# Optimization experiments

Hardware: AMD Instinct MI355X
Metric: run time of the kernel (lower is better)

Reference implementation:

```python
import jax, jax.numpy as jnp
import numpy as np

B, N, E, H = 8, 1024, 768, 12
HD = E // H

def setup_inputs() -> dict:
    key = jax.random.key(0)
    k1, k2, k3, k4, k5 = jax.random.split(key, 5)
    s = 0.02
    return {
        'query': jax.random.normal(k1, (B, N, E), dtype=jnp.float32),
        'qkv_w': jax.random.normal(k2, (3 * E, E), dtype=jnp.float32) * s,
        'qkv_b': jax.random.normal(k3, (3 * E,), dtype=jnp.float32) * s,
        'out_w': jax.random.normal(k4, (E, E), dtype=jnp.float32) * s,
        'out_b': jax.random.normal(k5, (E,), dtype=jnp.float32) * s,
    }

def reference(query, qkv_w, qkv_b, out_w, out_b):
    b, n, e = query.shape
    scale = HD ** -0.5
    # torch Linear: x @ W^T + b
    qkv = query @ qkv_w.T + qkv_b              # [B,N,3E]
    qkv = qkv.reshape(b, n, 3, H, HD)
    q = qkv[:, :, 0].transpose(0, 2, 1, 3)     # [B,H,N,hd]
    k = qkv[:, :, 1].transpose(0, 2, 1, 3)
    v = qkv[:, :, 2].transpose(0, 2, 1, 3)
    attn = jnp.einsum('bhqd,bhkd->bhqk', q, k) * scale
    attn = jax.nn.softmax(attn, axis=-1)
    x = jnp.einsum('bhqk,bhkd->bhqd', attn, v)  # [B,H,N,hd]
    x = x.transpose(0, 2, 1, 3).reshape(b, n, e)
    return x @ out_w.T + out_b
```

## Files before the change

### kernel.cpp

```cpp
#include <hip/hip_runtime.h>
#include <cstdint>
#include <cstddef>

#define QSCALE 0.18033688011112042f

typedef __bf16 bf16x8 __attribute__((ext_vector_type(8)));
typedef __bf16 bf16x4 __attribute__((ext_vector_type(4)));
typedef short short4v __attribute__((ext_vector_type(4)));
typedef float floatx4 __attribute__((ext_vector_type(4)));

static __device__ __forceinline__ uint16_t f2bf(float f) {
    uint32_t u = __builtin_bit_cast(uint32_t, f);
    u += 0x7FFFu + ((u >> 16) & 1u);
    return (uint16_t)(u >> 16);
}

static __device__ __forceinline__ void st_bf16(uint16_t* p, float f) {
    *(__bf16*)p = (__bf16)f;
}

static __device__ __forceinline__ bf16x8 ld_frag(const uint16_t* p) {
    uint4 u = *(const uint4*)p;
    return __builtin_bit_cast(bf16x8, u);
}

static __device__ __forceinline__ void async_lds16(const uint16_t* g, uint16_t* l) {
    __builtin_amdgcn_global_load_lds(
        (const __attribute__((address_space(1))) void*)g,
        (__attribute__((address_space(3))) void*)l,
        16, 0, 0);
}

static __device__ __forceinline__ size_t qk_swz(int bh, int idx, int hd) {
    return (size_t)bh * 65536 + (size_t)(idx >> 4) * 1024 + (size_t)(hd >> 5) * 512
         + (size_t)((hd & 31) >> 3) * 128 + (size_t)(idx & 15) * 8 + (hd & 7);
}
static __device__ __forceinline__ size_t v_swz(int bh, int hd, int key) {
    return (size_t)bh * 65536 + (size_t)(key >> 6) * 4096 + (size_t)(hd >> 4) * 1024
         + (size_t)((key >> 4) & 3) * 256 + (size_t)((key >> 2) & 3) * 64
         + (size_t)(hd & 15) * 4 + (key & 3);
}

__global__ __launch_bounds__(256) void cast3_kernel(
    const float* __restrict__ a, uint16_t* __restrict__ da, int na8,
    const float* __restrict__ b, uint16_t* __restrict__ db, int nb8,
    const float* __restrict__ c, uint16_t* __restrict__ dc, int nc8)
{
    int i = blockIdx.x * 256 + threadIdx.x;
    const float* src; uint16_t* dst; int idx;
    if (i < na8)                { src = a; dst = da; idx = i; }
    else if (i < na8 + nb8)     { src = b; dst = db; idx = i - na8; }
    else if (i < na8 + nb8 + nc8){ src = c; dst = dc; idx = i - na8 - nb8; }
    else return;
    const float4* p = (const float4*)src + (size_t)2 * idx;
    float4 x = p[0], y = p[1];
    uint32_t w0 = (uint32_t)f2bf(x.x) | ((uint32_t)f2bf(x.y) << 16);
    uint32_t w1 = (uint32_t)f2bf(x.z) | ((uint32_t)f2bf(x.w) << 16);
    uint32_t w2 = (uint32_t)f2bf(y.x) | ((uint32_t)f2bf(y.y) << 16);
    uint32_t w3 = (uint32_t)f2bf(y.z) | ((uint32_t)f2bf(y.w) << 16);
    uint4 v; v.x = w0; v.y = w1; v.z = w2; v.w = w3;
    *((uint4*)dst + idx) = v;
}

__global__ __launch_bounds__(256) void gemm_qkv_kernel(
    const uint16_t* __restrict__ X,
    const uint16_t* __restrict__ W,
    const float* __restrict__ bias,
    uint16_t* __restrict__ Qs, uint16_t* __restrict__ Ks, uint16_t* __restrict__ Vs)
{
    __shared__ __align__(16) uint16_t As[128 * 32];
    __shared__ __align__(16) uint16_t Bs[128 * 32];
    const int tid = threadIdx.x;
    const int wave = tid >> 6, lane = tid & 63;
    const int L = lane & 15, quad = lane >> 4;
    const int wM = (wave >> 1) * 64, wN = (wave & 1) * 64;
    const int bm = blockIdx.x * 128;
    const int bn = blockIdx.y * 128;

    floatx4 zero4 = {0.f, 0.f, 0.f, 0.f};
    floatx4 acc[4][4];
    #pragma unroll
    for (int i = 0; i < 4; ++i)
        #pragma unroll
        for (int j = 0; j < 4; ++j) acc[i][j] = zero4;

    const int srow = tid >> 2;
    const int scol = ((tid & 3) ^ ((srow >> 1) & 3)) * 8;
    const uint16_t* xp0 = X + (size_t)(bm + srow) * 768 + scol;
    const uint16_t* xp1 = xp0 + (size_t)64 * 768;
    const uint16_t* wp0 = W + (size_t)(bn + srow) * 768 + scol;
    const uint16_t* wp1 = wp0 + (size_t)64 * 768;
    uint16_t* lA0 = As + wave * 512;
    uint16_t* lA1 = As + 2048 + wave * 512;
    uint16_t* lB0 = Bs + wave * 512;
    uint16_t* lB1 = Bs + 2048 + wave * 512;

    const int cq = (quad ^ ((L >> 1) & 3)) * 8;

    for (int k0 = 0; k0 < 768; k0 += 32) {
        __syncthreads();
        async_lds16(xp0 + k0, lA0);
        async_lds16(xp1 + k0, lA1);
        async_lds16(wp0 + k0, lB0);
        async_lds16(wp1 + k0, lB1);
        __syncthreads();
        bf16x8 af[4], bfr[4];
        #pragma unroll
        for (int mi = 0; mi < 4; ++mi) af[mi]  = ld_frag(&As[(wM + mi * 16 + L) * 32 + cq]);
        #pragma unroll
        for (int ni = 0; ni < 4; ++ni) bfr[ni] = ld_frag(&Bs[(wN + ni * 16 + L) * 32 + cq]);
        #pragma unroll
        for (int mi = 0; mi < 4; ++mi)
            #pragma unroll
            for (int ni = 0; ni < 4; ++ni)
                acc[mi][ni] = __builtin_amdgcn_mfma_f32_16x16x32_bf16(
                    af[mi], bfr[ni], acc[mi][ni], 0, 0, 0);
    }

    const int part = bn / 768;
    #pragma unroll
    for (int ni = 0; ni < 4; ++ni) {
        int col = bn + wN + ni * 16 + L;
        int c = col - part * 768;
        int h = c >> 6, hd = c & 63;
        float bv = bias[col];
        #pragma unroll
        for (int mi = 0; mi < 4; ++mi) {
            #pragma unroll
            for (int r = 0; r < 4; ++r) {
                int m = bm + wM + mi * 16 + quad * 4 + r;
                int b = m >> 10, ns = m & 1023;
                int bh = b * 12 + h;
                float v = acc[mi][ni][r] + bv;
                if (part == 0)      st_bf16(&Qs[qk_swz(bh, ns, hd)], v * QSCALE);
                else if (part == 1) st_bf16(&Ks[qk_swz(bh, ns, hd)], v);
                else                st_bf16(&Vs[v_swz(bh, hd, ns)], v);
            }
        }
    }
}

__global__ __launch_bounds__(256) void attn_kernel(
    const uint16_t* __restrict__ Qs,
    const uint16_t* __restrict__ Ks,
    const uint16_t* __restrict__ Vs,
    uint16_t* __restrict__ Ob)
{
    __shared__ __align__(16) uint16_t Ksh[4096];
    __shared__ __align__(16) uint16_t Vsh[4096];
    const int tid = threadIdx.x;
    const int wave = tid >> 6, lane = tid & 63;
    const int L = lane & 15, quad = lane >> 4;
    const int bh = blockIdx.x;
    const int qt = blockIdx.y;
    const int b = bh / 12, h = bh - b * 12;
    const int q0 = qt * 128 + wave * 32;

    floatx4 zero4 = {0.f, 0.f, 0.f, 0.f};

    const uint16_t* qbase = Qs + (size_t)bh * 65536 + (size_t)lane * 8;
    bf16x8 aq[2][2];
    #pragma unroll
    for (int st = 0; st < 2; ++st) {
        const uint16_t* qp = qbase + (size_t)(qt * 8 + wave * 2 + st) * 1024;
        aq[st][0] = ld_frag(qp);
        aq[st][1] = ld_frag(qp + 512);
    }

    floatx4 accO[2][4];
    #pragma unroll
    for (int st = 0; st < 2; ++st)
        #pragma unroll
        for (int t = 0; t < 4; ++t) accO[st][t] = zero4;
    float lacc[2] = {0.f, 0.f};

    const uint16_t* ktile0 = Ks + (size_t)bh * 65536;
    const uint16_t* vtile0 = Vs + (size_t)bh * 65536;
    const size_t lane8 = (size_t)lane * 8;

    for (int j = 0; j < 16; ++j) {
        __syncthreads();
        const uint16_t* kt = ktile0 + (size_t)j * 4096;
        const uint16_t* vt = vtile0 + (size_t)j * 4096;
        async_lds16(kt + (size_t)wave * 512 + lane8,       Ksh + wave * 512);
        async_lds16(kt + (size_t)(wave + 4) * 512 + lane8, Ksh + (wave + 4) * 512);
        async_lds16(vt + (size_t)wave * 512 + lane8,       Vsh + wave * 512);
        async_lds16(vt + (size_t)(wave + 4) * 512 + lane8, Vsh + (wave + 4) * 512);
        __syncthreads();

        bf16x8 ka[4][2];
        #pragma unroll
        for (int kc = 0; kc < 4; ++kc) {
            ka[kc][0] = ld_frag(&Ksh[kc * 1024 + lane * 8]);
            ka[kc][1] = ld_frag(&Ksh[kc * 1024 + 512 + lane * 8]);
        }
        short4v va[4][4];
        #pragma unroll
        for (int t = 0; t < 4; ++t)
            #pragma unroll
            for (int kc = 0; kc < 4; ++kc)
                va[kc][t] = *(const short4v*)(&Vsh[t * 1024 + kc * 256 + lane * 4]);

        floatx4 c[2][4];
        #pragma unroll
        for (int st = 0; st < 2; ++st)
            #pragma unroll
            for (int kc = 0; kc < 4; ++kc) {
                floatx4 z = zero4;
                z = __builtin_amdgcn_mfma_f32_16x16x32_bf16(ka[kc][0], aq[st][0], z, 0, 0, 0);
                z = __builtin_amdgcn_mfma_f32_16x16x32_bf16(ka[kc][1], aq[st][1], z, 0, 0, 0);
                c[st][kc] = z;
            }

        short4v pb[2][4];
        #pragma unroll
        for (int st = 0; st < 2; ++st)
            #pragma unroll
            for (int kc = 0; kc < 4; ++kc) {
                float p0 = __builtin_amdgcn_exp2f(c[st][kc][0]);
                float p1 = __builtin_amdgcn_exp2f(c[st][kc][1]);
                float p2 = __builtin_amdgcn_exp2f(c[st][kc][2]);
                float p3 = __builtin_amdgcn_exp2f(c[st][kc][3]);
                lacc[st] += (p0 + p1) + (p2 + p3);
                bf16x4 t4;
                t4.x = (__bf16)p0; t4.y = (__bf16)p1;
                t4.z = (__bf16)p2; t4.w = (__bf16)p3;
                pb[st][kc] = __builtin_bit_cast(short4v, t4);
            }

        #pragma unroll
        for (int st = 0; st < 2; ++st)
            #pragma unroll
            for (int t = 0; t < 4; ++t)
                #pragma unroll
                for (int kc = 0; kc < 4; ++kc)
                    accO[st][t] = __builtin_amdgcn_mfma_f32_16x16x16bf16_1k(
                        va[kc][t], pb[st][kc], accO[st][t], 0, 0, 0);
    }

    #pragma unroll
    for (int st = 0; st < 2; ++st) {
        float sum = lacc[st];
        sum += __shfl_xor(sum, 16);
        sum += __shfl_xor(sum, 32);
        float inv = 1.f / sum;
        uint16_t* orow = Ob + ((size_t)b * 1024 + q0 + st * 16 + L) * 768 + h * 64 + quad * 4;
        #pragma unroll
        for (int t = 0; t < 4; ++t) {
            bf16x4 o4;
            o4.x = (__bf16)(accO[st][t][0] * inv);
            o4.y = (__bf16)(accO[st][t][1] * inv);
            o4.z = (__bf16)(accO[st][t][2] * inv);
            o4.w = (__bf16)(accO[st][t][3] * inv);
            *(uint2*)(orow + t * 16) = __builtin_bit_cast(uint2, o4);
        }
    }
}

__global__ __launch_bounds__(256) void gemm_out_kernel(
    const uint16_t* __restrict__ X,
    const uint16_t* __restrict__ W,
    const float* __restrict__ bias,
    float* __restrict__ out)
{
    __shared__ __align__(16) uint16_t As[128 * 32];
    __shared__ __align__(16) uint16_t Bs[64 * 32];
    const int tid = threadIdx.x;
    const int wave = tid >> 6, lane = tid & 63;
    const int L = lane & 15, quad = lane >> 4;
    const int wM = (wave >> 1) * 64, wN = (wave & 1) * 32;
    const int bm = blockIdx.x * 128;
    const int bn = blockIdx.y * 64;

    floatx4 zero4 = {0.f, 0.f, 0.f, 0.f};
    floatx4 acc[4][2];
    #pragma unroll
    for (int i = 0; i < 4; ++i)
        #pragma unroll
        for (int j = 0; j < 2; ++j) acc[i][j] = zero4;

    const int srow = tid >> 2;
    const int scol = ((tid & 3) ^ ((srow >> 1) & 3)) * 8;
    const uint16_t* xp0 = X + (size_t)(bm + srow) * 768 + scol;
    const uint16_t* xp1 = xp0 + (size_t)64 * 768;
    const uint16_t* wp0 = W + (size_t)(bn + srow) * 768 + scol;
    uint16_t* lA0 = As + wave * 512;
    uint16_t* lA1 = As + 2048 + wave * 512;
    uint16_t* lB0 = Bs + wave * 512;

    const int cq = (quad ^ ((L >> 1) & 3)) * 8;

    for (int k0 = 0; k0 < 768; k0 += 32) {
        __syncthreads();
        async_lds16(xp0 + k0, lA0);
        async_lds16(xp1 + k0, lA1);
        async_lds16(wp0 + k0, lB0);
        __syncthreads();
        bf16x8 af[4], bfr[2];
        #pragma unroll
        for (int mi = 0; mi < 4; ++mi) af[mi]  = ld_frag(&As[(wM + mi * 16 + L) * 32 + cq]);
        #pragma unroll
        for (int ni = 0; ni < 2; ++ni) bfr[ni] = ld_frag(&Bs[(wN + ni * 16 + L) * 32 + cq]);
        #pragma unroll
        for (int mi = 0; mi < 4; ++mi)
            #pragma unroll
            for (int ni = 0; ni < 2; ++ni)
                acc[mi][ni] = __builtin_amdgcn_mfma_f32_16x16x32_bf16(
                    af[mi], bfr[ni], acc[mi][ni], 0, 0, 0);
    }

    #pragma unroll
    for (int ni = 0; ni < 2; ++ni) {
        int col = bn + wN + ni * 16 + L;
        float bv = bias[col];
        #pragma unroll
        for (int mi = 0; mi < 4; ++mi)
            #pragma unroll
            for (int r = 0; r < 4; ++r) {
                int m = bm + wM + mi * 16 + quad * 4 + r;
                out[(size_t)m * 768 + col] = acc[mi][ni][r] + bv;
            }
    }
}

extern "C" void kernel_launch(void* const* d_in, const int* in_sizes, int n_in,
                              void* d_out, int out_size, void* d_ws, size_t ws_size,
                              hipStream_t stream) {
    const float* query = (const float*)d_in[0];
    const float* qkv_w = (const float*)d_in[1];
    const float* qkv_b = (const float*)d_in[2];
    const float* out_w = (const float*)d_in[3];
    const float* out_b = (const float*)d_in[4];
    float* out = (float*)d_out;

    uint8_t* ws = (uint8_t*)d_ws;
    uint16_t* Xb  = (uint16_t*)(ws);
    uint16_t* W1b = (uint16_t*)(ws + 12582912);
    uint16_t* W2b = (uint16_t*)(ws + 16121856);
    uint16_t* Qsw = (uint16_t*)(ws + 17301504);
    uint16_t* Ksw = (uint16_t*)(ws + 29884416);
    uint16_t* Vsw = (uint16_t*)(ws + 42467328);
    uint16_t* Ab  = Xb;

    cast3_kernel<<<4224, 256, 0, stream>>>(query, Xb, 786432,
                                           qkv_w, W1b, 221184,
                                           out_w, W2b, 73728);
    gemm_qkv_kernel<<<dim3(64, 18), 256, 0, stream>>>(Xb, W1b, qkv_b, Qsw, Ksw, Vsw);
    attn_kernel<<<dim3(96, 8), 256, 0, stream>>>(Qsw, Ksw, Vsw, Ab);
    gemm_out_kernel<<<dim3(64, 12), 256, 0, stream>>>(Ab, W2b, out_b, out);
}
```

Measured before the change: 190.5 us.

## Double-buffer K/V tiles in attention with async LDS prefetch

The attention loop now uses two LDS buffers for K and V. The next tile is issued with async global-to-LDS loads while the current tile is computed, and hand-off uses manual vmcnt/lgkmcnt waits with raw s_barrier instead of two __syncthreads per iteration. The goal is to hide global-load latency behind the MFMA work. The QKV GEMM also gains a min-blocks-per-CU launch bound of 4, which pushes the compiler to limit register use for occupancy. The cost is twice the LDS footprint in the attention kernel. The hand-tuned vmcnt(8) threshold is also a correctness risk if each staging call issues only four load instructions.

```diff
diff --git a/kernel.cpp b/kernel.cpp
--- a/kernel.cpp
+++ b/kernel.cpp
@@ -8,6 +8,10 @@
 typedef __bf16 bf16x4 __attribute__((ext_vector_type(4)));
 typedef short short4v __attribute__((ext_vector_type(4)));
 typedef float floatx4 __attribute__((ext_vector_type(4)));
+
+#define WAITVM8()   asm volatile("s_waitcnt vmcnt(8)" ::: "memory")
+#define WAITVM0()   asm volatile("s_waitcnt vmcnt(0)" ::: "memory")
+#define WAITLGKM0() asm volatile("s_waitcnt lgkmcnt(0)" ::: "memory")
 
 static __device__ __forceinline__ uint16_t f2bf(float f) {
     uint32_t u = __builtin_bit_cast(uint32_t, f);
@@ -62,7 +66,7 @@
     *((uint4*)dst + idx) = v;
 }
 
-__global__ __launch_bounds__(256) void gemm_qkv_kernel(
+__global__ __launch_bounds__(256, 4) void gemm_qkv_kernel(
     const uint16_t* __restrict__ X,
     const uint16_t* __restrict__ W,
     const float* __restrict__ bias,
@@ -140,14 +144,81 @@
     }
 }
 
+static __device__ __forceinline__ void stage_kv(
+    const uint16_t* kt, const uint16_t* vt, uint16_t* Kd, uint16_t* Vd,
+    int wave, size_t lane8)
+{
+    async_lds16(kt + (size_t)wave * 512 + lane8,       Kd + wave * 512);
+    async_lds16(kt + (size_t)(wave + 4) * 512 + lane8, Kd + (wave + 4) * 512);
+    async_lds16(vt + (size_t)wave * 512 + lane8,       Vd + wave * 512);
+    async_lds16(vt + (size_t)(wave + 4) * 512 + lane8, Vd + (wave + 4) * 512);
+}
+
+static __device__ __forceinline__ void attn_compute_tile(
+    const uint16_t* __restrict__ Ksh, const uint16_t* __restrict__ Vsh,
+    int lane, const bf16x8 (&aq)[2][2], floatx4 (&accO)[2][4], float (&lacc)[2])
+{
+    floatx4 zero4 = {0.f, 0.f, 0.f, 0.f};
+    bf16x8 ka[4][2];
+    #pragma unroll
+    for (int kc = 0; kc < 4; ++kc) {
+        ka[kc][0] = ld_frag(&Ksh[kc * 1024 + lane * 8]);
+        ka[kc][1] = ld_frag(&Ksh[kc * 1024 + 512 + lane * 8]);
+    }
+    short4v va[4][4];
+    #pragma unroll
+    for (int t = 0; t < 4; ++t)
+        #pragma unroll
+        for (int kc = 0; kc < 4; ++kc)
+            va[kc][t] = *(const short4v*)(&Vsh[t * 1024 + kc * 256 + lane * 4]);
+    WAITLGKM0();
+    __builtin_amdgcn_s_barrier();
+
+    floatx4 c[2][4];
+    #pragma unroll
+    for (int st = 0; st < 2; ++st)
+        #pragma unroll
+        for (int kc = 0; kc < 4; ++kc) {
+            floatx4 z = zero4;
+            z = __builtin_amdgcn_mfma_f32_16x16x32_bf16(ka[kc][0], aq[st][0], z, 0, 0, 0);
+            z = __builtin_amdgcn_mfma_f32_16x16x32_bf16(ka[kc][1], aq[st][1], z, 0, 0, 0);
+            c[st][kc] = z;
+        }
+
+    short4v pb[2][4];
+    #pragma unroll
+    for (int st = 0; st < 2; ++st)
+        #pragma unroll
+        for (int kc = 0; kc < 4; ++kc) {
+            float p0 = __builtin_amdgcn_exp2f(c[st][kc][0]);
+            float p1 = __builtin_amdgcn_exp2f(c[st][kc][1]);
+            float p2 = __builtin_amdgcn_exp2f(c[st][kc][2]);
+            float p3 = __builtin_amdgcn_exp2f(c[st][kc][3]);
+            lacc[st] += (p0 + p1) + (p2 + p3);
+            bf16x4 t4;
+            t4.x = (__bf16)p0; t4.y = (__bf16)p1;
+            t4.z = (__bf16)p2; t4.w = (__bf16)p3;
+            pb[st][kc] = __builtin_bit_cast(short4v, t4);
+        }
+
+    #pragma unroll
+    for (int st = 0; st < 2; ++st)
+        #pragma unroll
+        for (int t = 0; t < 4; ++t)
+            #pragma unroll
+            for (int kc = 0; kc < 4; ++kc)
+                accO[st][t] = __builtin_amdgcn_mfma_f32_16x16x16bf16_1k(
+                    va[kc][t], pb[st][kc], accO[st][t], 0, 0, 0);
+}
+
 __global__ __launch_bounds__(256) void attn_kernel(
     const uint16_t* __restrict__ Qs,
     const uint16_t* __restrict__ Ks,
     const uint16_t* __restrict__ Vs,
     uint16_t* __restrict__ Ob)
 {
-    __shared__ __align__(16) uint16_t Ksh[4096];
-    __shared__ __align__(16) uint16_t Vsh[4096];
+    __shared__ __align__(16) uint16_t Ksh[2][4096];
+    __shared__ __align__(16) uint16_t Vsh[2][4096];
     const int tid = threadIdx.x;
     const int wave = tid >> 6, lane = tid & 63;
     const int L = lane & 15, quad = lane >> 4;
@@ -178,64 +249,25 @@
     const uint16_t* vtile0 = Vs + (size_t)bh * 65536;
     const size_t lane8 = (size_t)lane * 8;
 
-    for (int j = 0; j < 16; ++j) {
-        __syncthreads();
-        const uint16_t* kt = ktile0 + (size_t)j * 4096;
-        const uint16_t* vt = vtile0 + (size_t)j * 4096;
-        async_lds16(kt + (size_t)wave * 512 + lane8,       Ksh + wave * 512);
-        async_lds16(kt + (size_t)(wave + 4) * 512 + lane8, Ksh + (wave + 4) * 512);
-        async_lds16(vt + (size_t)wave * 512 + lane8,       Vsh + wave * 512);
-        async_lds16(vt + (size_t)(wave + 4) * 512 + lane8, Vsh + (wave + 4) * 512);
-        __syncthreads();
-
-        bf16x8 ka[4][2];
-        #pragma unroll
-        for (int kc = 0; kc < 4; ++kc) {
-            ka[kc][0] = ld_frag(&Ksh[kc * 1024 + lane * 8]);
-            ka[kc][1] = ld_frag(&Ksh[kc * 1024 + 512 + lane * 8]);
-        }
-        short4v va[4][4];
-        #pragma unroll
-        for (int t = 0; t < 4; ++t)
-            #pragma unroll
-            for (int kc = 0; kc < 4; ++kc)
-                va[kc][t] = *(const short4v*)(&Vsh[t * 1024 + kc * 256 + lane * 4]);
-
-        floatx4 c[2][4];
-        #pragma unroll
-        for (int st = 0; st < 2; ++st)
-            #pragma unroll
-            for (int kc = 0; kc < 4; ++kc) {
-                floatx4 z = zero4;
-                z = __builtin_amdgcn_mfma_f32_16x16x32_bf16(ka[kc][0], aq[st][0], z, 0, 0, 0);
-                z = __builtin_amdgcn_mfma_f32_16x16x32_bf16(ka[kc][1], aq[st][1], z, 0, 0, 0);
-                c[st][kc] = z;
-            }
-
-        short4v pb[2][4];
-        #pragma unroll
-        for (int st = 0; st < 2; ++st)
-            #pragma unroll
-            for (int kc = 0; kc < 4; ++kc) {
-                float p0 = __builtin_amdgcn_exp2f(c[st][kc][0]);
-                float p1 = __builtin_amdgcn_exp2f(c[st][kc][1]);
-                float p2 = __builtin_amdgcn_exp2f(c[st][kc][2]);
-                float p3 = __builtin_amdgcn_exp2f(c[st][kc][3]);
-                lacc[st] += (p0 + p1) + (p2 + p3);
-                bf16x4 t4;
-                t4.x = (__bf16)p0; t4.y = (__bf16)p1;
-                t4.z = (__bf16)p2; t4.w = (__bf16)p3;
-                pb[st][kc] = __builtin_bit_cast(short4v, t4);
-            }
-
-        #pragma unroll
-        for (int st = 0; st < 2; ++st)
-            #pragma unroll
-            for (int t = 0; t < 4; ++t)
-                #pragma unroll
-                for (int kc = 0; kc < 4; ++kc)
-                    accO[st][t] = __builtin_amdgcn_mfma_f32_16x16x16bf16_1k(
-                        va[kc][t], pb[st][kc], accO[st][t], 0, 0, 0);
+    stage_kv(ktile0, vtile0, Ksh[0], Vsh[0], wave, lane8);
+
+    #pragma unroll 1
+    for (int jj = 0; jj < 8; ++jj) {
+        const int j0 = jj * 2;
+        stage_kv(ktile0 + (size_t)(j0 + 1) * 4096, vtile0 + (size_t)(j0 + 1) * 4096,
+                 Ksh[1], Vsh[1], wave, lane8);
+        WAITVM8();
+        __builtin_amdgcn_s_barrier();
+        attn_compute_tile(Ksh[0], Vsh[0], lane, aq, accO, lacc);
+        if (jj < 7) {
+            stage_kv(ktile0 + (size_t)(j0 + 2) * 4096, vtile0 + (size_t)(j0 + 2) * 4096,
+                     Ksh[0], Vsh[0], wave, lane8);
+            WAITVM8();
+        } else {
+            WAITVM0();
+        }
+        __builtin_amdgcn_s_barrier();
+        attn_compute_tile(Ksh[1], Vsh[1], lane, aq, accO, lacc);
     }
 
     #pragma unroll
```

Measured after the change: 197.3 us. +3.6%, slower.

## Pre-swizzle QKV weight into MFMA fragment order and load B directly to registers

Applied to the files above, without the earlier changes.

The cast kernel now writes the QKV weight in an MFMA fragment-ordered layout, one 64-lane fragment per 16 rows by 32 k-slice. The QKV GEMM loads B fragments straight from global memory into registers, prefetching the next k-step, so the B shared-memory tile and its LDS traffic are gone. This frees LDS and lowers shared-memory bandwidth use, but B now comes from global or L2 per wave, with redundancy across the two M-waves. The cast kernel's weight reads become strided rather than contiguous.

```diff
diff --git a/kernel.cpp b/kernel.cpp
--- a/kernel.cpp
+++ b/kernel.cpp
@@ -47,12 +47,20 @@
     const float* __restrict__ c, uint16_t* __restrict__ dc, int nc8)
 {
     int i = blockIdx.x * 256 + threadIdx.x;
-    const float* src; uint16_t* dst; int idx;
-    if (i < na8)                { src = a; dst = da; idx = i; }
-    else if (i < na8 + nb8)     { src = b; dst = db; idx = i - na8; }
-    else if (i < na8 + nb8 + nc8){ src = c; dst = dc; idx = i - na8 - nb8; }
+    const float* src; uint16_t* dst; int idx; int swz;
+    if (i < na8)                { src = a; dst = da; idx = i; swz = 0; }
+    else if (i < na8 + nb8)     { src = b; dst = db; idx = i - na8; swz = 1; }
+    else if (i < na8 + nb8 + nc8){ src = c; dst = dc; idx = i - na8 - nb8; swz = 0; }
     else return;
-    const float4* p = (const float4*)src + (size_t)2 * idx;
+    size_t srcElem;
+    if (swz) {
+        int frag = idx >> 6, ln = idx & 63;
+        int m16 = frag / 24, kt = frag - m16 * 24;
+        srcElem = (size_t)(m16 * 16 + (ln & 15)) * 768 + kt * 32 + (ln >> 4) * 8;
+    } else {
+        srcElem = (size_t)idx * 8;
+    }
+    const float4* p = (const float4*)(src + srcElem);
     float4 x = p[0], y = p[1];
     uint32_t w0 = (uint32_t)f2bf(x.x) | ((uint32_t)f2bf(x.y) << 16);
     uint32_t w1 = (uint32_t)f2bf(x.z) | ((uint32_t)f2bf(x.w) << 16);
@@ -64,12 +72,11 @@
 
 __global__ __launch_bounds__(256) void gemm_qkv_kernel(
     const uint16_t* __restrict__ X,
-    const uint16_t* __restrict__ W,
+    const uint16_t* __restrict__ Wf,
     const float* __restrict__ bias,
     uint16_t* __restrict__ Qs, uint16_t* __restrict__ Ks, uint16_t* __restrict__ Vs)
 {
     __shared__ __align__(16) uint16_t As[128 * 32];
-    __shared__ __align__(16) uint16_t Bs[128 * 32];
     const int tid = threadIdx.x;
     const int wave = tid >> 6, lane = tid & 63;
     const int L = lane & 15, quad = lane >> 4;
@@ -88,33 +95,39 @@
     const int scol = ((tid & 3) ^ ((srow >> 1) & 3)) * 8;
     const uint16_t* xp0 = X + (size_t)(bm + srow) * 768 + scol;
     const uint16_t* xp1 = xp0 + (size_t)64 * 768;
-    const uint16_t* wp0 = W + (size_t)(bn + srow) * 768 + scol;
-    const uint16_t* wp1 = wp0 + (size_t)64 * 768;
     uint16_t* lA0 = As + wave * 512;
     uint16_t* lA1 = As + 2048 + wave * 512;
-    uint16_t* lB0 = Bs + wave * 512;
-    uint16_t* lB1 = Bs + 2048 + wave * 512;
 
     const int cq = (quad ^ ((L >> 1) & 3)) * 8;
 
-    for (int k0 = 0; k0 < 768; k0 += 32) {
-        __syncthreads();
+    const uint16_t* bb = Wf + (size_t)((bn + wN) >> 4) * (24 * 512) + (size_t)lane * 8;
+
+    bf16x8 bcur[4], bnxt[4];
+    #pragma unroll
+    for (int ni = 0; ni < 4; ++ni) bcur[ni] = ld_frag(bb + (size_t)(ni * 24) * 512);
+
+    for (int t = 0; t < 24; ++t) {
+        __syncthreads();
+        const int k0 = t * 32;
         async_lds16(xp0 + k0, lA0);
         async_lds16(xp1 + k0, lA1);
-        async_lds16(wp0 + k0, lB0);
-        async_lds16(wp1 + k0, lB1);
-        __syncthreads();
-        bf16x8 af[4], bfr[4];
-        #pragma unroll
-        for (int mi = 0; mi < 4; ++mi) af[mi]  = ld_frag(&As[(wM + mi * 16 + L) * 32 + cq]);
-        #pragma unroll
-        for (int ni = 0; ni < 4; ++ni) bfr[ni] = ld_frag(&Bs[(wN + ni * 16 + L) * 32 + cq]);
+        __syncthreads();
+        if (t < 23) {
+            #pragma unroll
+            for (int ni = 0; ni < 4; ++ni)
+                bnxt[ni] = ld_frag(bb + (size_t)(ni * 24 + t + 1) * 512);
+        }
+        bf16x8 af[4];
+        #pragma unroll
+        for (int mi = 0; mi < 4; ++mi) af[mi] = ld_frag(&As[(wM + mi * 16 + L) * 32 + cq]);
         #pragma unroll
         for (int mi = 0; mi < 4; ++mi)
             #pragma unroll
             for (int ni = 0; ni < 4; ++ni)
                 acc[mi][ni] = __builtin_amdgcn_mfma_f32_16x16x32_bf16(
-                    af[mi], bfr[ni], acc[mi][ni], 0, 0, 0);
+                    af[mi], bcur[ni], acc[mi][ni], 0, 0, 0);
+        #pragma unroll
+        for (int ni = 0; ni < 4; ++ni) bcur[ni] = bnxt[ni];
     }
 
     const int part = bn / 768;
```

Result: slower. 197.1 us (+3.5%).
